# Kernel optimization log

Measured on AMD Instinct MI355X. Metric: run time of the kernel, lower is better.

## Reference

```python
import jax, jax.numpy as jnp
import numpy as np
import math

N_HEAD = 16


def _causal_attn(q, k, v):
    # q: [B,H,L,d], k/v: [B,H,S,d]; standard scaled-dot-product causal attention
    d_k = q.shape[-1]
    s = jnp.einsum('bhqd,bhkd->bhqk', q, k) / math.sqrt(d_k)
    L, S = q.shape[-2], k.shape[-2]
    mask = jnp.tril(jnp.ones((L, S), dtype=bool))
    s = jnp.where(mask, s, -jnp.inf)
    a = jax.nn.softmax(s, axis=-1)
    return jnp.einsum('bhqk,bhkd->bhqd', a, v)


def setup_inputs() -> dict:
    key = jax.random.key(0)
    ks = jax.random.split(key, 8)
    B, T, C = 2, 2048, 1024
    scale = 0.02
    return {
        'x': jax.random.normal(ks[0], (B, T, C), dtype=jnp.float32),
        'W_attn': jax.random.normal(ks[1], (C, 2 * C), dtype=jnp.float32) * scale,
        'b_attn': jnp.zeros((2 * C,), dtype=jnp.float32),
        'W_k2': jax.random.normal(ks[2], (C, C), dtype=jnp.float32) * scale,
        'b_k2': jnp.zeros((C,), dtype=jnp.float32),
        'W_proj': jax.random.normal(ks[3], (C, C), dtype=jnp.float32) * scale,
        'b_proj': jnp.zeros((C,), dtype=jnp.float32),
    }


def reference(x, W_attn, b_attn, W_k2, b_k2, W_proj, b_proj):
    # Eval-mode forward of CausalSelfAttentionARMA (all dropouts inactive).
    B, T, C = x.shape
    H = N_HEAD
    d = C // H

    qk = x @ W_attn + b_attn                      # [B,T,2C]
    q, k = qk[..., :C], qk[..., C:]
    q = q.reshape(B, T, H, d).transpose(0, 2, 1, 3)   # [B,H,T,d]
    k = k.reshape(B, T, H, d).transpose(0, 2, 1, 3)
    v = x.reshape(B, T, H, d).transpose(0, 2, 1, 3)   # v = x (no value proj)

    # AR pass: standard causal attention
    y = _causal_attn(q, k, v)                     # [B,H,T,d]

    # MA residual: e_t = v_{t+1} - y_t
    e = v[:, :, 1:, :] - y[:, :, :-1, :]          # [B,H,T-1,d]

    k2 = (x[:, :-1] @ W_k2 + b_k2).reshape(B, T - 1, H, d).transpose(0, 2, 1, 3)
    q2 = q[:, :, 1:, :]

    # MA pass: second causal attention over residuals
    y2 = _causal_attn(q2, k2, e)                  # [B,H,T-1,d]
    y2 = jnp.concatenate([jnp.zeros_like(y2[:, :, :1, :]), y2], axis=2)  # [B,H,T,d]

    def proj(t):
        return t.transpose(0, 2, 1, 3).reshape(B, T, C) @ W_proj + b_proj

    return proj(y) + proj(y2)
```

## Files before the change

### kernel.cpp

```cpp
#include <hip/hip_runtime.h>
#include <hip/hip_bf16.h>

typedef unsigned short u16;
typedef short s16x8 __attribute__((ext_vector_type(8)));
typedef float f32x4 __attribute__((ext_vector_type(4)));

#define LOG2E 1.44269504088896f

__device__ __forceinline__ u16 f2b(float f){
    __hip_bfloat16 h = __float2bfloat16(f);
    return __builtin_bit_cast(unsigned short, h);
}
__device__ __forceinline__ float b2f(u16 u){
    __hip_bfloat16 h = __builtin_bit_cast(__hip_bfloat16, u);
    return __bfloat162float(h);
}
__device__ __forceinline__ unsigned int pk2(float a, float b){
    return (unsigned int)f2b(a) | ((unsigned int)f2b(b) << 16);
}

__global__ void k_f32_to_bf16(const float* __restrict__ in, u16* __restrict__ out, int n4){
    int i = blockIdx.x*blockDim.x + threadIdx.x;
    int stride = gridDim.x*blockDim.x;
    for (; i < n4; i += stride){
        float4 a = *(const float4*)&in[(size_t)i*4];
        uint2 o;
        o.x = pk2(a.x, a.y);
        o.y = pk2(a.z, a.w);
        *(uint2*)&out[(size_t)i*4] = o;
    }
}

__global__ void k_transpose_bf16(const float* __restrict__ W, u16* __restrict__ Wt, int K, int N){
    __shared__ float tile[32][33];
    int n0 = blockIdx.x*32, k0 = blockIdx.y*32;
    int c = threadIdx.x & 31, r0 = threadIdx.x >> 5;
#pragma unroll
    for (int it = 0; it < 4; ++it){
        int r = r0 + it*8;
        tile[r][c] = W[(size_t)(k0+r)*N + n0 + c];
    }
    __syncthreads();
#pragma unroll
    for (int it = 0; it < 4; ++it){
        int r = r0 + it*8;
        Wt[(size_t)(n0+r)*K + k0 + c] = f2b(tile[c][r]);
    }
}

__global__ __launch_bounds__(256) void k_build_vT(const float* __restrict__ x, u16* __restrict__ VT){
    __shared__ float tile[64][65];
    int bh = blockIdx.x, t0 = blockIdx.y*64;
    int b = bh >> 4, h = bh & 15;
    int tid = threadIdx.x;
    {
        int tt = tid >> 2, ds = (tid & 3)*16;
        const float* xp = &x[((size_t)(b*2048) + t0 + tt)*1024 + h*64 + ds];
#pragma unroll
        for (int j4 = 0; j4 < 4; ++j4){
            float4 a = *(const float4*)&xp[j4*4];
            tile[tt][ds + j4*4 + 0] = a.x;
            tile[tt][ds + j4*4 + 1] = a.y;
            tile[tt][ds + j4*4 + 2] = a.z;
            tile[tt][ds + j4*4 + 3] = a.w;
        }
    }
    __syncthreads();
    {
        int dd = tid >> 2, ts = (tid & 3)*16;
        unsigned int o[8];
#pragma unroll
        for (int j = 0; j < 8; ++j)
            o[j] = pk2(tile[ts + 2*j][dd], tile[ts + 2*j + 1][dd]);
        u16* dst = &VT[((size_t)(bh*64 + dd))*2048 + t0 + ts];
        *(uint4*)&dst[0] = *(uint4*)&o[0];
        *(uint4*)&dst[8] = *(uint4*)&o[4];
    }
}

__global__ __launch_bounds__(256) void k_compute_eT(const float* __restrict__ x, const float* __restrict__ y1,
                                                    u16* __restrict__ ET){
    __shared__ float tile[64][65];
    int bh = blockIdx.x, j0 = blockIdx.y*64;
    int b = bh >> 4, h = bh & 15;
    int tid = threadIdx.x;
    {
        int tt = tid >> 2, ds = (tid & 3)*16;
        int j = j0 + tt; if (j > 2046) j = 2046;
        const float* xp = &x[((size_t)(b*2048) + j + 1)*1024 + h*64 + ds];
        const float* yp = &y1[((size_t)bh*2048 + j)*64 + ds];
#pragma unroll
        for (int j4 = 0; j4 < 4; ++j4){
            float4 a = *(const float4*)&xp[j4*4];
            float4 c = *(const float4*)&yp[j4*4];
            tile[tt][ds + j4*4 + 0] = a.x - c.x;
            tile[tt][ds + j4*4 + 1] = a.y - c.y;
            tile[tt][ds + j4*4 + 2] = a.z - c.z;
            tile[tt][ds + j4*4 + 3] = a.w - c.w;
        }
    }
    __syncthreads();
    {
        int dd = tid >> 2, ts = (tid & 3)*16;
        unsigned int o[8];
#pragma unroll
        for (int j = 0; j < 8; ++j)
            o[j] = pk2(tile[ts + 2*j][dd], tile[ts + 2*j + 1][dd]);
        u16* dst = &ET[((size_t)(bh*64 + dd))*2048 + j0 + ts];
        *(uint4*)&dst[0] = *(uint4*)&o[0];
        *(uint4*)&dst[8] = *(uint4*)&o[4];
    }
}

template<int MODE>
__global__ __launch_bounds__(256) void k_gemm(const u16* __restrict__ A, const u16* __restrict__ Bt,
                       const float* __restrict__ bias, float* __restrict__ outF,
                       u16* __restrict__ out0, u16* __restrict__ out1,
                       int M, int N, int K){
    __shared__ u16 As[128][72];
    __shared__ u16 Bs[128][72];
    int m0 = blockIdx.y * 128, n0 = blockIdx.x * 128;
    int tid = threadIdx.x;
    int lane = tid & 63, w = tid >> 6;
    int wm = w >> 1, wn = w & 1;
    int l15 = lane & 15, l4 = lane >> 4;
    f32x4 acc[4][4] = {};

    for (int kt = 0; kt < K; kt += 64){
#pragma unroll
        for (int it = 0; it < 4; ++it){
            int c = tid + 256*it;
            int row = c >> 3, seg = c & 7;
            *(uint4*)&As[row][seg*8] = *(const uint4*)&A[(size_t)(m0+row)*K + kt + seg*8];
            *(uint4*)&Bs[row][seg*8] = *(const uint4*)&Bt[(size_t)(n0+row)*K + kt + seg*8];
        }
        __syncthreads();
#pragma unroll
        for (int kk = 0; kk < 2; ++kk){
            s16x8 a[4], b[4];
#pragma unroll
            for (int mi = 0; mi < 4; ++mi)
                a[mi] = *(const s16x8*)&As[wm*64 + mi*16 + l15][kk*32 + l4*8];
#pragma unroll
            for (int ni = 0; ni < 4; ++ni)
                b[ni] = *(const s16x8*)&Bs[wn*64 + ni*16 + l15][kk*32 + l4*8];
#pragma unroll
            for (int mi = 0; mi < 4; ++mi)
#pragma unroll
                for (int ni = 0; ni < 4; ++ni)
                    acc[mi][ni] = __builtin_amdgcn_mfma_f32_16x16x32_bf16(a[mi], b[ni], acc[mi][ni], 0,0,0);
        }
        __syncthreads();
    }

#pragma unroll
    for (int mi = 0; mi < 4; ++mi){
        int growb = m0 + wm*64 + mi*16 + l4*4;
#pragma unroll
        for (int ni = 0; ni < 4; ++ni){
            int gcol = n0 + wn*64 + ni*16 + l15;
            float bv = bias[gcol];
#pragma unroll
            for (int r = 0; r < 4; ++r){
                int row = growb + r;
                float val = acc[mi][ni][r];
                if (MODE == 2){
                    outF[(size_t)row*N + gcol] = val + 2.0f*bv;
                } else {
                    val += bv;
                    int bb = row >> 11, t = row & 2047;
                    if (MODE == 0){
                        if (gcol < 1024){
                            int h = gcol >> 6, dd = gcol & 63;
                            out0[(((size_t)(bb*16+h))*2048 + t)*64 + dd] = f2b(val*0.125f);
                        } else {
                            int c2 = gcol - 1024;
                            int h = c2 >> 6, dd = c2 & 63;
                            out1[(((size_t)(bb*16+h))*2048 + t)*64 + dd] = f2b(val);
                        }
                    } else {
                        int h = gcol >> 6, dd = gcol & 63;
                        out0[(((size_t)(bb*16+h))*2048 + t)*64 + dd] = f2b(val);
                    }
                }
            }
        }
    }
}

__global__ __launch_bounds__(256) void k_flash(const u16* __restrict__ Q, const u16* __restrict__ Km,
                        const u16* __restrict__ VT, float* __restrict__ O,
                        int Tq, int Tkv, int qstride, int kstride, int vtstride, int ostride, int qoff){
    __shared__ u16 Ks[64][72];
    __shared__ u16 VTs[64][72];
    __shared__ u16 Ps[64][72];
    int bh = blockIdx.x;
    int qt = (int)((blockIdx.y + blockIdx.x) & 31);
    int qs = qt * 64;
    int tid = threadIdx.x, lane = tid & 63, w = tid >> 6;
    int l15 = lane & 15, l4 = lane >> 4;
    const u16* Qp = Q + ((size_t)bh*qstride + qoff)*64;
    const u16* Kp = Km + (size_t)bh*kstride*64;
    const u16* Vp = VT + (size_t)bh*64*vtstride;

    s16x8 aq[2];
    {
        int qrow = qs + w*16 + l15; if (qrow > Tq-1) qrow = Tq-1;
        aq[0] = *(const s16x8*)&Qp[(size_t)qrow*64 + l4*8];
        aq[1] = *(const s16x8*)&Qp[(size_t)qrow*64 + 32 + l4*8];
    }
    f32x4 Of[4] = {};
    float m_r[4], l_r[4];
#pragma unroll
    for (int r = 0; r < 4; ++r){ m_r[r] = -INFINITY; l_r[r] = 0.f; }

    int nt = qt + 1;
    int srow = tid >> 2, sq4 = tid & 3;

    uint4 kr0, kr1, vr0, vr1;
    {
        int krow = 0 + srow; if (krow > Tkv-1) krow = Tkv-1;
        kr0 = *(const uint4*)&Kp[(size_t)krow*64 + sq4*16];
        kr1 = *(const uint4*)&Kp[(size_t)krow*64 + sq4*16 + 8];
        vr0 = *(const uint4*)&Vp[(size_t)srow*vtstride + 0 + sq4*16];
        vr1 = *(const uint4*)&Vp[(size_t)srow*vtstride + 0 + sq4*16 + 8];
    }

    for (int ti = 0; ti < nt; ++ti){
        int ks0 = ti*64;
        *(uint4*)&Ks[srow][sq4*16]      = kr0;
        *(uint4*)&Ks[srow][sq4*16 + 8]  = kr1;
        *(uint4*)&VTs[srow][sq4*16]     = vr0;
        *(uint4*)&VTs[srow][sq4*16 + 8] = vr1;
        __syncthreads();
        if (ti + 1 < nt){
            int ks1 = ks0 + 64;
            int krow = ks1 + srow; if (krow > Tkv-1) krow = Tkv-1;
            kr0 = *(const uint4*)&Kp[(size_t)krow*64 + sq4*16];
            kr1 = *(const uint4*)&Kp[(size_t)krow*64 + sq4*16 + 8];
            vr0 = *(const uint4*)&Vp[(size_t)srow*vtstride + ks1 + sq4*16];
            vr1 = *(const uint4*)&Vp[(size_t)srow*vtstride + ks1 + sq4*16 + 8];
        }
        f32x4 sf[4] = {};
#pragma unroll
        for (int kk = 0; kk < 2; ++kk)
#pragma unroll
            for (int ni = 0; ni < 4; ++ni){
                s16x8 bk = *(const s16x8*)&Ks[ni*16 + l15][kk*32 + l4*8];
                sf[ni] = __builtin_amdgcn_mfma_f32_16x16x32_bf16(aq[kk], bk, sf[ni], 0,0,0);
            }
        bool diag = (ti == nt - 1);
#pragma unroll
        for (int r = 0; r < 4; ++r){
            int grow = qs + w*16 + l4*4 + r;
            float mx = -INFINITY;
            if (diag){
#pragma unroll
                for (int ni = 0; ni < 4; ++ni){
                    int col = ks0 + ni*16 + l15;
                    float s = sf[ni][r];
                    if (col > grow || col >= Tkv) s = -INFINITY;
                    sf[ni][r] = s;
                    mx = fmaxf(mx, s);
                }
            } else {
#pragma unroll
                for (int ni = 0; ni < 4; ++ni) mx = fmaxf(mx, sf[ni][r]);
            }
            mx = fmaxf(mx, __shfl_xor(mx, 1));
            mx = fmaxf(mx, __shfl_xor(mx, 2));
            mx = fmaxf(mx, __shfl_xor(mx, 4));
            mx = fmaxf(mx, __shfl_xor(mx, 8));
            float mnew = fmaxf(m_r[r], mx);
            float scale = exp2f((m_r[r] - mnew)*LOG2E);
            float rs = 0.f;
#pragma unroll
            for (int ni = 0; ni < 4; ++ni){
                float p = exp2f((sf[ni][r] - mnew)*LOG2E);
                u16 pb = f2b(p);
                rs += b2f(pb);
                Ps[w*16 + l4*4 + r][ni*16 + l15] = pb;
            }
            rs += __shfl_xor(rs, 1);
            rs += __shfl_xor(rs, 2);
            rs += __shfl_xor(rs, 4);
            rs += __shfl_xor(rs, 8);
            l_r[r] = l_r[r]*scale + rs;
            m_r[r] = mnew;
#pragma unroll
            for (int di = 0; di < 4; ++di) Of[di][r] *= scale;
        }
#pragma unroll
        for (int kk = 0; kk < 2; ++kk){
            s16x8 ap = *(const s16x8*)&Ps[w*16 + l15][kk*32 + l4*8];
#pragma unroll
            for (int di = 0; di < 4; ++di){
                s16x8 bv = *(const s16x8*)&VTs[di*16 + l15][kk*32 + l4*8];
                Of[di] = __builtin_amdgcn_mfma_f32_16x16x32_bf16(ap, bv, Of[di], 0,0,0);
            }
        }
        __syncthreads();
    }
#pragma unroll
    for (int r = 0; r < 4; ++r){
        int grow = qs + w*16 + l4*4 + r;
        if (grow < Tq){
            float inv = 1.0f / l_r[r];
#pragma unroll
            for (int di = 0; di < 4; ++di)
                O[((size_t)bh*ostride + grow)*64 + di*16 + l15] = Of[di][r] * inv;
        }
    }
}

__global__ void k_ysum(const float* __restrict__ y1, const float* __restrict__ y2,
                       u16* __restrict__ ys){
    int i = blockIdx.x*blockDim.x + threadIdx.x;
    int stride = gridDim.x*blockDim.x;
    for (; i < (1<<20); i += stride){
        int d4 = i & 15;
        int t = (i >> 4) & 2047;
        int bh = i >> 15;
        float4 s = *(const float4*)&y1[(((size_t)bh*2048) + t)*64 + d4*4];
        if (t > 0){
            float4 z = *(const float4*)&y2[(((size_t)bh*2048) + t - 1)*64 + d4*4];
            s.x += z.x; s.y += z.y; s.z += z.z; s.w += z.w;
        }
        uint2 o;
        o.x = pk2(s.x, s.y);
        o.y = pk2(s.z, s.w);
        int bb = bh >> 4, hh = bh & 15;
        *(uint2*)&ys[(((size_t)bb*2048) + t)*1024 + hh*64 + d4*4] = o;
    }
}

extern "C" void kernel_launch(void* const* d_in, const int* in_sizes, int n_in,
                              void* d_out, int out_size, void* d_ws, size_t ws_size,
                              hipStream_t stream){
    const float* x      = (const float*)d_in[0];
    const float* W_attn = (const float*)d_in[1];
    const float* b_attn = (const float*)d_in[2];
    const float* W_k2   = (const float*)d_in[3];
    const float* b_k2   = (const float*)d_in[4];
    const float* W_proj = (const float*)d_in[5];
    const float* b_proj = (const float*)d_in[6];
    float* out = (float*)d_out;

    char* ws = (char*)d_ws;
    size_t off = 0;
    auto alloc = [&](size_t bytes)->void*{
        void* p = ws + off; off += (bytes + 255) & ~size_t(255); return p;
    };
    u16* xb   = (u16*)alloc((size_t)4096*1024*2);
    u16* WaT  = (u16*)alloc((size_t)2048*1024*2);
    u16* Wk2T = (u16*)alloc((size_t)1024*1024*2);
    u16* WpT  = (u16*)alloc((size_t)1024*1024*2);
    u16* Qb   = (u16*)alloc((size_t)32*2048*64*2);
    u16* Kb   = (u16*)alloc((size_t)32*2048*64*2);
    u16* VTg  = (u16*)alloc((size_t)32*64*2048*2);
    u16* K2b  = (u16*)alloc((size_t)32*2048*64*2);
    u16* ETg  = (u16*)alloc((size_t)32*64*2048*2);
    float* y1 = (float*)alloc((size_t)32*2048*64*4);
    float* y2 = (float*)alloc((size_t)32*2048*64*4);
    u16* ys   = (u16*)alloc((size_t)4096*1024*2);

    k_f32_to_bf16<<<1024, 256, 0, stream>>>(x, xb, 1<<20);
    k_transpose_bf16<<<dim3(64, 32), 256, 0, stream>>>(W_attn, WaT, 1024, 2048);
    k_transpose_bf16<<<dim3(32, 32), 256, 0, stream>>>(W_k2, Wk2T, 1024, 1024);
    k_transpose_bf16<<<dim3(32, 32), 256, 0, stream>>>(W_proj, WpT, 1024, 1024);
    k_build_vT<<<dim3(32, 32), 256, 0, stream>>>(x, VTg);

    k_gemm<0><<<dim3(16, 32), 256, 0, stream>>>(xb, WaT, b_attn, nullptr, Qb, Kb, 4096, 2048, 1024);
    k_gemm<1><<<dim3(8, 32), 256, 0, stream>>>(xb, Wk2T, b_k2, nullptr, K2b, nullptr, 4096, 1024, 1024);

    k_flash<<<dim3(32, 32), 256, 0, stream>>>(Qb, Kb, VTg, y1, 2048, 2048, 2048, 2048, 2048, 2048, 0);
    k_compute_eT<<<dim3(32, 32), 256, 0, stream>>>(x, y1, ETg);
    k_flash<<<dim3(32, 32), 256, 0, stream>>>(Qb, K2b, ETg, y2, 2047, 2047, 2048, 2048, 2048, 2048, 1);
    k_ysum<<<1024, 256, 0, stream>>>(y1, y2, ys);

    k_gemm<2><<<dim3(8, 32), 256, 0, stream>>>(ys, WpT, b_proj, out, nullptr, nullptr, 4096, 1024, 1024);
}
```

Baseline: 393.0 us.

## Rewrite flash attention with 32x32 MFMA, 128-row tiles, balanced causal pairing

Replaces the 16x16 MFMA flash kernel with one that uses 32x32x16 MFMA. Each block handles two 128-query tiles, paired as t and 15-t so the causal work per block is balanced. P is kept in registers and exchanged with lane shuffles instead of going through shared memory, K/V tiles use an XOR-swizzled layout, and the running-max rescale is skipped unless some row's max grows by more than 8. Outputs are written transposed (d-major), so k_compute_eT and k_ysum are changed to read that layout. The grid drops to 256 blocks, which may lower occupancy, and the lazy rescale trades some numerical headroom for fewer exponentials.

```diff
diff --git a/kernel.cpp b/kernel.cpp
--- a/kernel.cpp
+++ b/kernel.cpp
@@ -4,6 +4,8 @@
 typedef unsigned short u16;
 typedef short s16x8 __attribute__((ext_vector_type(8)));
 typedef float f32x4 __attribute__((ext_vector_type(4)));
+typedef float f32x16 __attribute__((ext_vector_type(16)));
+typedef unsigned int u32x4 __attribute__((ext_vector_type(4)));
 
 #define LOG2E 1.44269504088896f
 
@@ -78,7 +80,7 @@
     }
 }
 
-__global__ __launch_bounds__(256) void k_compute_eT(const float* __restrict__ x, const float* __restrict__ y1,
+__global__ __launch_bounds__(256) void k_compute_eT(const float* __restrict__ x, const float* __restrict__ y1T,
                                                     u16* __restrict__ ET){
     __shared__ float tile[64][65];
     int bh = blockIdx.x, j0 = blockIdx.y*64;
@@ -86,26 +88,30 @@
     int tid = threadIdx.x;
     {
         int tt = tid >> 2, ds = (tid & 3)*16;
-        int j = j0 + tt; if (j > 2046) j = 2046;
-        const float* xp = &x[((size_t)(b*2048) + j + 1)*1024 + h*64 + ds];
-        const float* yp = &y1[((size_t)bh*2048 + j)*64 + ds];
+        int j = j0 + tt;
+        int xr = (j <= 2046) ? (j + 1) : 2047;
+        const float* xp = &x[((size_t)(b*2048) + xr)*1024 + h*64 + ds];
 #pragma unroll
         for (int j4 = 0; j4 < 4; ++j4){
             float4 a = *(const float4*)&xp[j4*4];
-            float4 c = *(const float4*)&yp[j4*4];
-            tile[tt][ds + j4*4 + 0] = a.x - c.x;
-            tile[tt][ds + j4*4 + 1] = a.y - c.y;
-            tile[tt][ds + j4*4 + 2] = a.z - c.z;
-            tile[tt][ds + j4*4 + 3] = a.w - c.w;
+            tile[tt][ds + j4*4 + 0] = a.x;
+            tile[tt][ds + j4*4 + 1] = a.y;
+            tile[tt][ds + j4*4 + 2] = a.z;
+            tile[tt][ds + j4*4 + 3] = a.w;
         }
     }
     __syncthreads();
     {
         int dd = tid >> 2, ts = (tid & 3)*16;
+        const float* yp = &y1T[((size_t)(bh*64 + dd))*2048 + j0 + ts];
         unsigned int o[8];
 #pragma unroll
-        for (int j = 0; j < 8; ++j)
-            o[j] = pk2(tile[ts + 2*j][dd], tile[ts + 2*j + 1][dd]);
+        for (int j = 0; j < 8; ++j){
+            int c0 = ts + 2*j, c1 = ts + 2*j + 1;
+            float e0 = (j0 + c0 <= 2046) ? (tile[c0][dd] - yp[2*j])   : 0.f;
+            float e1 = (j0 + c1 <= 2046) ? (tile[c1][dd] - yp[2*j+1]) : 0.f;
+            o[j] = pk2(e0, e1);
+        }
         u16* dst = &ET[((size_t)(bh*64 + dd))*2048 + j0 + ts];
         *(uint4*)&dst[0] = *(uint4*)&o[0];
         *(uint4*)&dst[8] = *(uint4*)&o[4];
@@ -188,149 +194,183 @@
     }
 }
 
-__global__ __launch_bounds__(256) void k_flash(const u16* __restrict__ Q, const u16* __restrict__ Km,
-                        const u16* __restrict__ VT, float* __restrict__ O,
-                        int Tq, int Tkv, int qstride, int kstride, int vtstride, int ostride, int qoff){
-    __shared__ u16 Ks[64][72];
-    __shared__ u16 VTs[64][72];
-    __shared__ u16 Ps[64][72];
+__global__ __launch_bounds__(256) void k_flash32(const u16* __restrict__ Q, const u16* __restrict__ Km,
+                         const u16* __restrict__ VT, float* __restrict__ OT,
+                         int Tq, int Tkv, int qoff){
+    __shared__ u16 Ks[64*64];
+    __shared__ u16 Vs[64*64];
     int bh = blockIdx.x;
-    int qt = (int)((blockIdx.y + blockIdx.x) & 31);
-    int qs = qt * 64;
-    int tid = threadIdx.x, lane = tid & 63, w = tid >> 6;
-    int l15 = lane & 15, l4 = lane >> 4;
-    const u16* Qp = Q + ((size_t)bh*qstride + qoff)*64;
-    const u16* Kp = Km + (size_t)bh*kstride*64;
-    const u16* Vp = VT + (size_t)bh*64*vtstride;
-
-    s16x8 aq[2];
-    {
-        int qrow = qs + w*16 + l15; if (qrow > Tq-1) qrow = Tq-1;
-        aq[0] = *(const s16x8*)&Qp[(size_t)qrow*64 + l4*8];
-        aq[1] = *(const s16x8*)&Qp[(size_t)qrow*64 + 32 + l4*8];
-    }
-    f32x4 Of[4] = {};
-    float m_r[4], l_r[4];
-#pragma unroll
-    for (int r = 0; r < 4; ++r){ m_r[r] = -INFINITY; l_r[r] = 0.f; }
-
-    int nt = qt + 1;
-    int srow = tid >> 2, sq4 = tid & 3;
-
-    uint4 kr0, kr1, vr0, vr1;
-    {
-        int krow = 0 + srow; if (krow > Tkv-1) krow = Tkv-1;
-        kr0 = *(const uint4*)&Kp[(size_t)krow*64 + sq4*16];
-        kr1 = *(const uint4*)&Kp[(size_t)krow*64 + sq4*16 + 8];
-        vr0 = *(const uint4*)&Vp[(size_t)srow*vtstride + 0 + sq4*16];
-        vr1 = *(const uint4*)&Vp[(size_t)srow*vtstride + 0 + sq4*16 + 8];
-    }
-
-    for (int ti = 0; ti < nt; ++ti){
-        int ks0 = ti*64;
-        *(uint4*)&Ks[srow][sq4*16]      = kr0;
-        *(uint4*)&Ks[srow][sq4*16 + 8]  = kr1;
-        *(uint4*)&VTs[srow][sq4*16]     = vr0;
-        *(uint4*)&VTs[srow][sq4*16 + 8] = vr1;
+    int pair = blockIdx.y;
+    int tid = threadIdx.x;
+    int lane = tid & 63, w = tid >> 6;
+    int l31 = lane & 31, hi = lane >> 5;
+    const u16* Qp = Q + ((size_t)bh*2048 + qoff)*64;
+    const u16* Kp = Km + (size_t)bh*2048*64;
+    const u16* Vp = VT + (size_t)bh*64*2048;
+    float* Op = OT + (size_t)bh*64*2048;
+
+    int srow = tid >> 2;
+    int sc   = tid & 3;
+
+#pragma unroll 1
+    for (int half = 0; half < 2; ++half){
+        int t = half ? (15 - pair) : pair;
+        int ntile = 2*t + 2;
+        int q0w = t*128 + w*32;
+        int qi = q0w + l31; if (qi > Tq-1) qi = Tq-1;
+
+        s16x8 qf[4];
+#pragma unroll
+        for (int st = 0; st < 4; ++st)
+            qf[st] = *(const s16x8*)&Qp[(size_t)qi*64 + st*16 + hi*8];
+
+        f32x16 accO[2] = {};
+        float m_r = -INFINITY, l_r = 0.f;
+
+        uint4 kr0, kr1, vr0, vr1;
+        {
+            int kvr = srow; if (kvr > Tkv-1) kvr = Tkv-1;
+            kr0 = *(const uint4*)&Kp[(size_t)kvr*64 + sc*16];
+            kr1 = *(const uint4*)&Kp[(size_t)kvr*64 + sc*16 + 8];
+            vr0 = *(const uint4*)&Vp[(size_t)srow*2048 + sc*16];
+            vr1 = *(const uint4*)&Vp[(size_t)srow*2048 + sc*16 + 8];
+        }
+
+        for (int i = 0; i < ntile; ++i){
+            int kv0 = i*64;
+            {
+                int sw = srow & 7;
+                *(uint4*)&Ks[srow*64 + (((2*sc)   ^ sw)*8)] = kr0;
+                *(uint4*)&Ks[srow*64 + (((2*sc+1) ^ sw)*8)] = kr1;
+                *(uint4*)&Vs[srow*64 + (((2*sc)   ^ sw)*8)] = vr0;
+                *(uint4*)&Vs[srow*64 + (((2*sc+1) ^ sw)*8)] = vr1;
+            }
+            __syncthreads();
+            if (i + 1 < ntile){
+                int kv1 = kv0 + 64;
+                int kvr = kv1 + srow; if (kvr > Tkv-1) kvr = Tkv-1;
+                kr0 = *(const uint4*)&Kp[(size_t)kvr*64 + sc*16];
+                kr1 = *(const uint4*)&Kp[(size_t)kvr*64 + sc*16 + 8];
+                vr0 = *(const uint4*)&Vp[(size_t)srow*2048 + kv1 + sc*16];
+                vr1 = *(const uint4*)&Vp[(size_t)srow*2048 + kv1 + sc*16 + 8];
+            }
+            if (kv0 <= q0w + 31){
+                f32x16 accS[2] = {};
+#pragma unroll
+                for (int m = 0; m < 2; ++m){
+                    int row = 32*m + l31;
+                    int sw = row & 7;
+#pragma unroll
+                    for (int st = 0; st < 4; ++st){
+                        s16x8 a = *(const s16x8*)&Ks[row*64 + (((2*st + hi) ^ sw)*8)];
+                        accS[m] = __builtin_amdgcn_mfma_f32_32x32x16_bf16(a, qf[st], accS[m], 0,0,0);
+                    }
+                }
+                float p[32];
+                bool diag = (kv0 + 63 > q0w);
+#pragma unroll
+                for (int m = 0; m < 2; ++m)
+#pragma unroll
+                    for (int r = 0; r < 16; ++r){
+                        float s = accS[m][r];
+                        if (diag){
+                            int kg = kv0 + 32*m + (r&3) + 8*(r>>2) + 4*hi;
+                            if (kg > qi) s = -INFINITY;
+                        }
+                        p[m*16 + r] = s;
+                    }
+                float mx = p[0];
+#pragma unroll
+                for (int j = 1; j < 32; ++j) mx = fmaxf(mx, p[j]);
+                mx = fmaxf(mx, __shfl_xor(mx, 32));
+                float mnew = fmaxf(m_r, mx);
+                if (!__all(mx - m_r <= 8.f)){
+                    float scl = exp2f((m_r - mnew)*LOG2E);
+#pragma unroll
+                    for (int dt = 0; dt < 2; ++dt)
+#pragma unroll
+                        for (int r = 0; r < 16; ++r) accO[dt][r] *= scl;
+                    l_r *= scl;
+                    m_r = mnew;
+                }
+                float rs = 0.f;
+#pragma unroll
+                for (int j = 0; j < 32; ++j){
+                    p[j] = exp2f((p[j] - m_r)*LOG2E);
+                    rs += p[j];
+                }
+                rs += __shfl_xor(rs, 32);
+                l_r += rs;
+#pragma unroll
+                for (int m = 0; m < 2; ++m)
+#pragma unroll
+                    for (int s2 = 0; s2 < 2; ++s2){
+                        const float* pp = &p[m*16 + s2*8];
+                        unsigned dwa = pk2(pp[0], pp[1]);
+                        unsigned dwb = pk2(pp[2], pp[3]);
+                        unsigned dwc = pk2(pp[4], pp[5]);
+                        unsigned dwd = pk2(pp[6], pp[7]);
+                        unsigned xa = (unsigned)__shfl_xor((int)dwa, 32);
+                        unsigned xb = (unsigned)__shfl_xor((int)dwb, 32);
+                        unsigned xc = (unsigned)__shfl_xor((int)dwc, 32);
+                        unsigned xd = (unsigned)__shfl_xor((int)dwd, 32);
+                        u32x4 fv;
+                        fv.x = hi ? xc : dwa;
+                        fv.y = hi ? xd : dwb;
+                        fv.z = hi ? dwc : xa;
+                        fv.w = hi ? dwd : xb;
+                        s16x8 pf = __builtin_bit_cast(s16x8, fv);
+                        int vslot = m*4 + s2*2 + hi;
+#pragma unroll
+                        for (int dt = 0; dt < 2; ++dt){
+                            int vrow = dt*32 + l31;
+                            s16x8 va = *(const s16x8*)&Vs[vrow*64 + ((vslot ^ (vrow&7))*8)];
+                            accO[dt] = __builtin_amdgcn_mfma_f32_32x32x16_bf16(va, pf, accO[dt], 0,0,0);
+                        }
+                    }
+            }
+            __syncthreads();
+        }
+        float inv = 1.0f / l_r;
+#pragma unroll
+        for (int dt = 0; dt < 2; ++dt)
+#pragma unroll
+            for (int r = 0; r < 16; ++r){
+                int d = dt*32 + (r&3) + 8*(r>>2) + 4*hi;
+                Op[(size_t)d*2048 + qi] = accO[dt][r] * inv;
+            }
         __syncthreads();
-        if (ti + 1 < nt){
-            int ks1 = ks0 + 64;
-            int krow = ks1 + srow; if (krow > Tkv-1) krow = Tkv-1;
-            kr0 = *(const uint4*)&Kp[(size_t)krow*64 + sq4*16];
-            kr1 = *(const uint4*)&Kp[(size_t)krow*64 + sq4*16 + 8];
-            vr0 = *(const uint4*)&Vp[(size_t)srow*vtstride + ks1 + sq4*16];
-            vr1 = *(const uint4*)&Vp[(size_t)srow*vtstride + ks1 + sq4*16 + 8];
-        }
-        f32x4 sf[4] = {};
-#pragma unroll
-        for (int kk = 0; kk < 2; ++kk)
-#pragma unroll
-            for (int ni = 0; ni < 4; ++ni){
-                s16x8 bk = *(const s16x8*)&Ks[ni*16 + l15][kk*32 + l4*8];
-                sf[ni] = __builtin_amdgcn_mfma_f32_16x16x32_bf16(aq[kk], bk, sf[ni], 0,0,0);
-            }
-        bool diag = (ti == nt - 1);
-#pragma unroll
-        for (int r = 0; r < 4; ++r){
-            int grow = qs + w*16 + l4*4 + r;
-            float mx = -INFINITY;
-            if (diag){
-#pragma unroll
-                for (int ni = 0; ni < 4; ++ni){
-                    int col = ks0 + ni*16 + l15;
-                    float s = sf[ni][r];
-                    if (col > grow || col >= Tkv) s = -INFINITY;
-                    sf[ni][r] = s;
-                    mx = fmaxf(mx, s);
-                }
-            } else {
-#pragma unroll
-                for (int ni = 0; ni < 4; ++ni) mx = fmaxf(mx, sf[ni][r]);
-            }
-            mx = fmaxf(mx, __shfl_xor(mx, 1));
-            mx = fmaxf(mx, __shfl_xor(mx, 2));
-            mx = fmaxf(mx, __shfl_xor(mx, 4));
-            mx = fmaxf(mx, __shfl_xor(mx, 8));
-            float mnew = fmaxf(m_r[r], mx);
-            float scale = exp2f((m_r[r] - mnew)*LOG2E);
-            float rs = 0.f;
-#pragma unroll
-            for (int ni = 0; ni < 4; ++ni){
-                float p = exp2f((sf[ni][r] - mnew)*LOG2E);
-                u16 pb = f2b(p);
-                rs += b2f(pb);
-                Ps[w*16 + l4*4 + r][ni*16 + l15] = pb;
-            }
-            rs += __shfl_xor(rs, 1);
-            rs += __shfl_xor(rs, 2);
-            rs += __shfl_xor(rs, 4);
-            rs += __shfl_xor(rs, 8);
-            l_r[r] = l_r[r]*scale + rs;
-            m_r[r] = mnew;
-#pragma unroll
-            for (int di = 0; di < 4; ++di) Of[di][r] *= scale;
-        }
-#pragma unroll
-        for (int kk = 0; kk < 2; ++kk){
-            s16x8 ap = *(const s16x8*)&Ps[w*16 + l15][kk*32 + l4*8];
-#pragma unroll
-            for (int di = 0; di < 4; ++di){
-                s16x8 bv = *(const s16x8*)&VTs[di*16 + l15][kk*32 + l4*8];
-                Of[di] = __builtin_amdgcn_mfma_f32_16x16x32_bf16(ap, bv, Of[di], 0,0,0);
-            }
-        }
-        __syncthreads();
-    }
-#pragma unroll
-    for (int r = 0; r < 4; ++r){
-        int grow = qs + w*16 + l4*4 + r;
-        if (grow < Tq){
-            float inv = 1.0f / l_r[r];
-#pragma unroll
-            for (int di = 0; di < 4; ++di)
-                O[((size_t)bh*ostride + grow)*64 + di*16 + l15] = Of[di][r] * inv;
-        }
-    }
-}
-
-__global__ void k_ysum(const float* __restrict__ y1, const float* __restrict__ y2,
-                       u16* __restrict__ ys){
-    int i = blockIdx.x*blockDim.x + threadIdx.x;
-    int stride = gridDim.x*blockDim.x;
-    for (; i < (1<<20); i += stride){
-        int d4 = i & 15;
-        int t = (i >> 4) & 2047;
-        int bh = i >> 15;
-        float4 s = *(const float4*)&y1[(((size_t)bh*2048) + t)*64 + d4*4];
-        if (t > 0){
-            float4 z = *(const float4*)&y2[(((size_t)bh*2048) + t - 1)*64 + d4*4];
-            s.x += z.x; s.y += z.y; s.z += z.z; s.w += z.w;
-        }
-        uint2 o;
-        o.x = pk2(s.x, s.y);
-        o.y = pk2(s.z, s.w);
-        int bb = bh >> 4, hh = bh & 15;
-        *(uint2*)&ys[(((size_t)bb*2048) + t)*1024 + hh*64 + d4*4] = o;
+    }
+}
+
+__global__ __launch_bounds__(256) void k_ysum(const float* __restrict__ y1T, const float* __restrict__ y2T,
+                                              u16* __restrict__ ys){
+    __shared__ float tile[64][65];
+    int bh = blockIdx.x, t0 = blockIdx.y*64;
+    int b = bh >> 4, h = bh & 15;
+    int tid = threadIdx.x;
+    {
+        int dd = tid >> 2, ts = (tid & 3)*16;
+        const float* y1p = &y1T[((size_t)(bh*64 + dd))*2048 + t0 + ts];
+        const float* y2p = &y2T[((size_t)(bh*64 + dd))*2048 + t0 + ts - 1];
+#pragma unroll
+        for (int c = 0; c < 16; ++c){
+            int tg = t0 + ts + c;
+            float s = y1p[c];
+            if (tg > 0) s += y2p[c];
+            tile[ts + c][dd] = s;
+        }
+    }
+    __syncthreads();
+    {
+        int tt = tid >> 2, ds = (tid & 3)*16;
+        unsigned int o[8];
+#pragma unroll
+        for (int j = 0; j < 8; ++j)
+            o[j] = pk2(tile[tt][ds + 2*j], tile[tt][ds + 2*j + 1]);
+        u16* dst = &ys[((size_t)(b*2048) + t0 + tt)*1024 + h*64 + ds];
+        *(uint4*)&dst[0] = *(uint4*)&o[0];
+        *(uint4*)&dst[8] = *(uint4*)&o[4];
     }
 }
 
@@ -351,18 +391,18 @@
     auto alloc = [&](size_t bytes)->void*{
         void* p = ws + off; off += (bytes + 255) & ~size_t(255); return p;
     };
-    u16* xb   = (u16*)alloc((size_t)4096*1024*2);
-    u16* WaT  = (u16*)alloc((size_t)2048*1024*2);
-    u16* Wk2T = (u16*)alloc((size_t)1024*1024*2);
-    u16* WpT  = (u16*)alloc((size_t)1024*1024*2);
-    u16* Qb   = (u16*)alloc((size_t)32*2048*64*2);
-    u16* Kb   = (u16*)alloc((size_t)32*2048*64*2);
-    u16* VTg  = (u16*)alloc((size_t)32*64*2048*2);
-    u16* K2b  = (u16*)alloc((size_t)32*2048*64*2);
-    u16* ETg  = (u16*)alloc((size_t)32*64*2048*2);
-    float* y1 = (float*)alloc((size_t)32*2048*64*4);
-    float* y2 = (float*)alloc((size_t)32*2048*64*4);
-    u16* ys   = (u16*)alloc((size_t)4096*1024*2);
+    u16* xb    = (u16*)alloc((size_t)4096*1024*2);
+    u16* WaT   = (u16*)alloc((size_t)2048*1024*2);
+    u16* Wk2T  = (u16*)alloc((size_t)1024*1024*2);
+    u16* WpT   = (u16*)alloc((size_t)1024*1024*2);
+    u16* Qb    = (u16*)alloc((size_t)32*2048*64*2);
+    u16* Kb    = (u16*)alloc((size_t)32*2048*64*2);
+    u16* VTg   = (u16*)alloc((size_t)32*64*2048*2);
+    u16* K2b   = (u16*)alloc((size_t)32*2048*64*2);
+    u16* ETg   = (u16*)alloc((size_t)32*64*2048*2);
+    float* y1T = (float*)alloc((size_t)32*64*2048*4);
+    float* y2T = (float*)alloc((size_t)32*64*2048*4);
+    u16* ys    = (u16*)alloc((size_t)4096*1024*2);
 
     k_f32_to_bf16<<<1024, 256, 0, stream>>>(x, xb, 1<<20);
     k_transpose_bf16<<<dim3(64, 32), 256, 0, stream>>>(W_attn, WaT, 1024, 2048);
@@ -373,10 +413,10 @@
     k_gemm<0><<<dim3(16, 32), 256, 0, stream>>>(xb, WaT, b_attn, nullptr, Qb, Kb, 4096, 2048, 1024);
     k_gemm<1><<<dim3(8, 32), 256, 0, stream>>>(xb, Wk2T, b_k2, nullptr, K2b, nullptr, 4096, 1024, 1024);
 
-    k_flash<<<dim3(32, 32), 256, 0, stream>>>(Qb, Kb, VTg, y1, 2048, 2048, 2048, 2048, 2048, 2048, 0);
-    k_compute_eT<<<dim3(32, 32), 256, 0, stream>>>(x, y1, ETg);
-    k_flash<<<dim3(32, 32), 256, 0, stream>>>(Qb, K2b, ETg, y2, 2047, 2047, 2048, 2048, 2048, 2048, 1);
-    k_ysum<<<1024, 256, 0, stream>>>(y1, y2, ys);
+    k_flash32<<<dim3(32, 8), 256, 0, stream>>>(Qb, Kb, VTg, y1T, 2048, 2048, 0);
+    k_compute_eT<<<dim3(32, 32), 256, 0, stream>>>(x, y1T, ETg);
+    k_flash32<<<dim3(32, 8), 256, 0, stream>>>(Qb, K2b, ETg, y2T, 2047, 2047, 1);
+    k_ysum<<<dim3(32, 32), 256, 0, stream>>>(y1T, y2T, ys);
 
     k_gemm<2><<<dim3(8, 32), 256, 0, stream>>>(ys, WpT, b_proj, out, nullptr, nullptr, 4096, 1024, 1024);
 }
```

Result: faster. 355.6 us (-9.5%).
